# Performance work log

Measured on AMD Instinct MI355X. Metric: run time of the kernel, lower is better.

## Reference

```python
import jax, jax.numpy as jnp
import numpy as np

D_MODEL = 2048
D_STATE = 128
D_CONV = 4
EXPAND = 2
D_HEAD = 64
D_INNER = EXPAND * D_MODEL          # 4096 (= d_ssm, n_groups=1)
N_HEADS = D_INNER // D_HEAD         # 64
CONV_DIM = D_INNER + 2 * D_STATE    # 4352
D_IN_PROJ = 2 * D_INNER + 2 * D_STATE + N_HEADS  # 8512
CHUNK = 256
EPS = 1e-5


def setup_inputs() -> dict:
    key = jax.random.key(0)
    ks = jax.random.split(key, 8)
    B, L = 2, 4096
    u = jax.random.normal(ks[0], (B, L, D_MODEL), jnp.float32)
    W_in = 0.02 * jax.random.normal(ks[1], (D_IN_PROJ, D_MODEL), jnp.float32)
    conv_w = 0.1 * jax.random.normal(ks[2], (CONV_DIM, D_CONV), jnp.float32)
    conv_b = jnp.zeros((CONV_DIM,), jnp.float32)
    # dt_bias init: dt ~ exp(U*(log(.1)-log(.001)) + log(.001)); inv softplus
    dt = jnp.exp(jax.random.uniform(ks[3], (N_HEADS,)) * (np.log(0.1) - np.log(0.001)) + np.log(0.001))
    dt = jnp.clip(dt, 1e-4, None)
    dt_bias = dt + jnp.log(-jnp.expm1(-dt))
    A_log = jnp.log(jax.random.uniform(ks[4], (N_HEADS,), minval=1.0, maxval=16.0))
    Dp = jnp.ones((N_HEADS,), jnp.float32)
    norm_w = jnp.ones((D_INNER,), jnp.float32)
    W_out = 0.02 * jax.random.normal(ks[5], (D_MODEL, D_INNER), jnp.float32)
    return {"u": u, "W_in": W_in, "conv_w": conv_w, "conv_b": conv_b,
            "dt_bias": dt_bias, "A_log": A_log, "Dp": Dp, "norm_w": norm_w, "W_out": W_out}


def _forward(u, W_in, conv_w, conv_b, dt_bias, A_log, Dp, norm_w, W_out):
    b, l, _ = u.shape
    zxbcdt = u @ W_in.T                                   # [b,l,d_in_proj]
    z = zxbcdt[..., :D_INNER]                             # gate
    xBC = zxbcdt[..., D_INNER:D_INNER + CONV_DIM]
    dt = zxbcdt[..., D_INNER + CONV_DIM:]                 # [b,l,h]

    # depthwise causal conv1d + silu
    xpad = jnp.pad(xBC, ((0, 0), (D_CONV - 1, 0), (0, 0)))
    xBC = sum(xpad[:, w:w + l, :] * conv_w[:, w] for w in range(D_CONV)) + conv_b
    xBC = jax.nn.silu(xBC)

    x = xBC[..., :D_INNER]
    Bm = xBC[..., D_INNER:D_INNER + D_STATE]              # [b,l,n]
    Cm = xBC[..., D_INNER + D_STATE:]                     # [b,l,n]

    dt = jax.nn.softplus(dt + dt_bias)                    # [b,l,h]
    A = -jnp.exp(A_log)                                   # [h], negative

    c = l // CHUNK
    dtc = dt.reshape(b, c, CHUNK, h_ := N_HEADS)          # [b,c,s,h]
    dA_cs = jnp.cumsum(dtc * A, axis=2)                   # [b,c,s,h]
    xc = x.reshape(b, c, CHUNK, N_HEADS, D_HEAD)          # [b,c,s,h,p]
    Bc = Bm.reshape(b, c, CHUNK, D_STATE)                 # [b,c,s,n]
    Cc = Cm.reshape(b, c, CHUNK, D_STATE)

    # intra-chunk ("diagonal") term
    mask = jnp.tril(jnp.ones((CHUNK, CHUNK), bool))
    diff = dA_cs[:, :, :, None, :] - dA_cs[:, :, None, :, :]      # [b,c,i,j,h]
    L = jnp.exp(jnp.where(mask[None, None, :, :, None], diff, -jnp.inf))
    CB = jnp.einsum('bcin,bcjn->bcij', Cc, Bc)
    M = CB[..., None] * L * dtc[:, :, None, :, :]                 # [b,c,i,j,h]
    y_diag = jnp.einsum('bcijh,bcjhp->bcihp', M, xc)

    # per-chunk final states and inter-chunk scan
    decay_last = jnp.exp(dA_cs[:, :, -1:, :] - dA_cs)             # [b,c,s,h]
    states = jnp.einsum('bcsh,bcsn,bcshp->bchpn', decay_last * dtc, Bc, xc)
    chunk_decay = jnp.exp(dA_cs[:, :, -1, :])                     # [b,c,h]

    def step(s, inp):
        st, dec = inp
        return s * dec[:, :, None, None] + st, s

    s0 = jnp.zeros((b, N_HEADS, D_HEAD, D_STATE), u.dtype)
    _, prev = jax.lax.scan(step, s0, (states.transpose(1, 0, 2, 3, 4),
                                      chunk_decay.transpose(1, 0, 2)))
    prev = prev.transpose(1, 0, 2, 3, 4)                          # [b,c,h,p,n]

    y_off = jnp.einsum('bcin,bchpn,bcih->bcihp', Cc, prev, jnp.exp(dA_cs))

    y = y_diag + y_off + Dp[None, None, None, :, None] * xc       # [b,c,s,h,p]
    y = y.reshape(b, l, D_INNER)

    # gated RMSNorm (norm_before_gate=False): normalize(y * silu(z)) * w
    yg = y * jax.nn.silu(z)
    yg = yg * jax.lax.rsqrt(jnp.mean(yg * yg, axis=-1, keepdims=True) + EPS)
    y = yg * norm_w
    return y @ W_out.T                                            # [b,l,d_model]


def reference(u, W_in, conv_w, conv_b, dt_bias, A_log, Dp, norm_w, W_out):
    return _forward(u, W_in, conv_w, conv_b, dt_bias, A_log, Dp, norm_w, W_out)
```

## Files before the change

### kernel.cpp

```cpp
#include <hip/hip_runtime.h>
#include <hip/hip_bf16.h>

typedef long long ll;
typedef unsigned int uint;
typedef unsigned short ushort;

typedef __bf16 bf16x8 __attribute__((ext_vector_type(8)));
typedef float f32x4 __attribute__((ext_vector_type(4)));


__device__ __forceinline__ float silu_f(float x) { return x / (1.0f + expf(-x)); }
__device__ __forceinline__ float softplus_f(float x) {
  return x > 20.0f ? x : log1pf(expf(x));
}
__device__ __forceinline__ float b2f(ushort u) {
  return __uint_as_float(((uint)u) << 16);
}
__device__ __forceinline__ ushort f2b(float f) {
  uint x = __float_as_uint(f);
  return (ushort)((x + 0x7FFFu + ((x >> 16) & 1u)) >> 16);
}
__device__ __forceinline__ uint pk2(float a, float b) {
  return (uint)f2b(a) | ((uint)f2b(b) << 16);
}
__device__ __forceinline__ void unpack8(uint4 u, float* f) {
  f[0] = b2f((ushort)(u.x & 0xffff)); f[1] = b2f((ushort)(u.x >> 16));
  f[2] = b2f((ushort)(u.y & 0xffff)); f[3] = b2f((ushort)(u.y >> 16));
  f[4] = b2f((ushort)(u.z & 0xffff)); f[5] = b2f((ushort)(u.z >> 16));
  f[6] = b2f((ushort)(u.w & 0xffff)); f[7] = b2f((ushort)(u.w >> 16));
}
__device__ __forceinline__ void unpack8u(uint4 u, ushort* e) {
  e[0] = (ushort)(u.x & 0xffff); e[1] = (ushort)(u.x >> 16);
  e[2] = (ushort)(u.y & 0xffff); e[3] = (ushort)(u.y >> 16);
  e[4] = (ushort)(u.z & 0xffff); e[5] = (ushort)(u.z >> 16);
  e[6] = (ushort)(u.w & 0xffff); e[7] = (ushort)(u.w >> 16);
}

#define GLDS16(g, l)                                                     \
  __builtin_amdgcn_global_load_lds(                                      \
      (const __attribute__((address_space(1))) void*)(g),                \
      (__attribute__((address_space(3))) void*)(l), 16, 0, 0)

__global__ __launch_bounds__(256) void f32_to_bf16(
    const float* __restrict__ in, ushort* __restrict__ out, ll n)
{
  ll i = ((ll)blockIdx.x * 256 + threadIdx.x) * 8;
  if (i + 8 > n) return;
  float4 a = *(const float4*)&in[i];
  float4 b = *(const float4*)&in[i + 4];
  ushort4 o0; o0.x = f2b(a.x); o0.y = f2b(a.y); o0.z = f2b(a.z); o0.w = f2b(a.w);
  ushort4 o1; o1.x = f2b(b.x); o1.y = f2b(b.y); o1.z = f2b(b.z); o1.w = f2b(b.w);
  *(ushort4*)&out[i] = o0;
  *(ushort4*)&out[i + 4] = o1;
}

template <int CBF>
__global__ __launch_bounds__(256) void gemm_mfma(
    const ushort* __restrict__ A, const ushort* __restrict__ B, void* __restrict__ C,
    int Nreal, int K, int lda, int ldb, int ldc,
    ll batchA, ll batchB, ll batchC)
{
  A += (ll)blockIdx.z * batchA;
  B += (ll)blockIdx.z * batchB;
  __shared__ ushort As[128 * 32];
  __shared__ ushort Bs[128 * 32];
  const int t = threadIdx.x;
  const int lane = t & 63, w = t >> 6;
  const int wr = w >> 1, wc = w & 1;
  const int bm = blockIdx.y * 128, bn = blockIdx.x * 128;

  const int srow = t >> 2, skc = (t & 3) << 3;
  const ll a0 = (ll)(bm + srow) * lda + skc;
  const ll a1 = (ll)(bm + 64 + srow) * lda + skc;
  int br0 = bn + srow;      if (br0 >= Nreal) br0 = Nreal - 1;
  int br1 = bn + 64 + srow; if (br1 >= Nreal) br1 = Nreal - 1;
  const ll b0 = (ll)br0 * ldb + skc;
  const ll b1 = (ll)br1 * ldb + skc;
  ushort* lA0 = As + t * 8;        ushort* lA1 = As + 2048 + t * 8;
  ushort* lB0 = Bs + t * 8;        ushort* lB1 = Bs + 2048 + t * 8;

  f32x4 acc[4][4];
#pragma unroll
  for (int m = 0; m < 4; ++m)
#pragma unroll
    for (int n = 0; n < 4; ++n) acc[m][n] = (f32x4){0.f, 0.f, 0.f, 0.f};

  const int fr = lane & 15;
  const int fk = (lane >> 4) << 3;

  for (int k0 = 0; k0 < K; k0 += 32) {
    GLDS16(A + a0 + k0, lA0);
    GLDS16(A + a1 + k0, lA1);
    GLDS16(B + b0 + k0, lB0);
    GLDS16(B + b1 + k0, lB1);
    __syncthreads();
    bf16x8 af[4], bf[4];
#pragma unroll
    for (int m = 0; m < 4; ++m)
      af[m] = *(const bf16x8*)&As[(wr * 64 + m * 16 + fr) * 32 + fk];
#pragma unroll
    for (int n = 0; n < 4; ++n)
      bf[n] = *(const bf16x8*)&Bs[(wc * 64 + n * 16 + fr) * 32 + fk];
#pragma unroll
    for (int m = 0; m < 4; ++m)
#pragma unroll
      for (int n = 0; n < 4; ++n)
        acc[m][n] = __builtin_amdgcn_mfma_f32_16x16x32_bf16(af[m], bf[n], acc[m][n], 0, 0, 0);
    __syncthreads();
  }

  const int cr = (lane >> 4) << 2, cc = lane & 15;
  const ll zc = (ll)blockIdx.z * batchC;
#pragma unroll
  for (int m = 0; m < 4; ++m) {
#pragma unroll
    for (int n = 0; n < 4; ++n) {
#pragma unroll
      for (int j = 0; j < 4; ++j) {
        ll row = bm + wr * 64 + m * 16 + cr + j;
        int col = bn + wc * 64 + n * 16 + cc;
        if constexpr (CBF)
          ((ushort*)C)[zc + row * ldc + col] = f2b(acc[m][n][j]);
        else
          ((float*)C)[zc + row * ldc + col] = acc[m][n][j];
      }
    }
  }
}

__global__ __launch_bounds__(256) void conv_silu(
    const ushort* __restrict__ zx, const float* __restrict__ cw,
    const float* __restrict__ cbias, ushort* __restrict__ out)
{
  ll tid = (ll)blockIdx.x * 256 + threadIdx.x;
  int ch4 = (int)(tid % 1088) << 2;
  ll bl = tid / 1088;
  int l = (int)(bl & 4095);
  ll rowbase = bl - l;
  float4 acc = *(const float4*)&cbias[ch4];
  float4 w0 = *(const float4*)&cw[(ch4 + 0) * 4];
  float4 w1 = *(const float4*)&cw[(ch4 + 1) * 4];
  float4 w2 = *(const float4*)&cw[(ch4 + 2) * 4];
  float4 w3 = *(const float4*)&cw[(ch4 + 3) * 4];
#define TAP(W, COMP)                                                               \
  { int llx = l + (W) - 3;                                                         \
    if (llx >= 0) {                                                                \
      ushort4 xv = *(const ushort4*)&zx[(rowbase + llx) * 8576 + 4096 + ch4];      \
      acc.x = fmaf(b2f(xv.x), w0.COMP, acc.x);                                     \
      acc.y = fmaf(b2f(xv.y), w1.COMP, acc.y);                                     \
      acc.z = fmaf(b2f(xv.z), w2.COMP, acc.z);                                     \
      acc.w = fmaf(b2f(xv.w), w3.COMP, acc.w); } }
  TAP(0, x) TAP(1, y) TAP(2, z) TAP(3, w)
#undef TAP
  ushort4 o;
  o.x = f2b(silu_f(acc.x)); o.y = f2b(silu_f(acc.y));
  o.z = f2b(silu_f(acc.z)); o.w = f2b(silu_f(acc.w));
  *(ushort4*)&out[bl * 4352 + ch4] = o;
}

__global__ __launch_bounds__(256) void dt_cumsum(
    const ushort* __restrict__ zx, const float* __restrict__ dt_bias,
    const float* __restrict__ A_log, float* __restrict__ dt_sp,
    float* __restrict__ dA)
{
  __shared__ float sdt[256][64];
  const int bc = blockIdx.x;
  const int t = threadIdx.x;
#pragma unroll
  for (int q = 0; q < 16; ++q) {
    int ff = q * 256 + t;
    int i = ff >> 4;
    int h4 = (ff & 15) << 2;
    ushort4 v4 = *(const ushort4*)&zx[((ll)bc * 256 + i) * 8576 + 8448 + h4];
    float4 bb = *(const float4*)&dt_bias[h4];
    float4 v;
    v.x = softplus_f(b2f(v4.x) + bb.x); v.y = softplus_f(b2f(v4.y) + bb.y);
    v.z = softplus_f(b2f(v4.z) + bb.z); v.w = softplus_f(b2f(v4.w) + bb.w);
    *(float4*)&dt_sp[((ll)bc * 256 + i) * 64 + h4] = v;
    *(float4*)&sdt[i][h4] = v;
  }
  __syncthreads();
  if (t < 64) {
    const int h = t;
    const float Ah = -expf(A_log[h]);
    float run = 0.0f;
    for (int i = 0; i < 256; ++i) {
      run = fmaf(sdt[i][h], Ah, run);
      dA[((ll)bc * 256 + i) * 64 + h] = run;
    }
  }
}

__global__ __launch_bounds__(256) void bt_transpose(
    const ushort* __restrict__ xbc, ushort* __restrict__ BT)
{
  const int bc = blockIdx.x;
  const int st0 = blockIdx.y * 64;
  const int nt0 = blockIdx.z * 64;
  const int t = threadIdx.x;
  const int s_loc = t & 63, strip = t >> 6;
  const int nb = nt0 + strip * 16;
  const ll row = (ll)(bc * 256 + st0 + s_loc) * 4352 + 4096 + nb;
  uint4 v0 = *(const uint4*)&xbc[row];
  uint4 v1 = *(const uint4*)&xbc[row + 8];
  ushort e[16];
  unpack8u(v0, e); unpack8u(v1, e + 8);
#pragma unroll
  for (int k = 0; k < 16; ++k)
    BT[((ll)bc * 128 + nb + k) * 256 + st0 + s_loc] = e[k];
}

__global__ __launch_bounds__(256) void states_mfma(
    const ushort* __restrict__ xbc, const float* __restrict__ dt_sp,
    const float* __restrict__ dA, const ushort* __restrict__ BT,
    ushort* __restrict__ st)
{
  const int bc = blockIdx.x, h = blockIdx.y;
  const int t = threadIdx.x, lane = t & 63, w = t >> 6;
  __shared__ ushort xwT[64][264];
  const float dAl = dA[((ll)bc * 256 + 255) * 64 + h];
  const float wloc = expf(dAl - dA[((ll)bc * 256 + t) * 64 + h]) *
                     dt_sp[((ll)bc * 256 + t) * 64 + h];
  {
    const ll xrow = ((ll)bc * 256 + t) * 4352 + h * 64;
#pragma unroll
    for (int g = 0; g < 8; ++g) {
      uint4 v = *(const uint4*)&xbc[xrow + g * 8];
      float f[8]; unpack8(v, f);
#pragma unroll
      for (int j = 0; j < 8; ++j)
        xwT[g * 8 + j][t] = f2b(f[j] * wloc);
    }
  }
  __syncthreads();

  const int fr = lane & 15, fk = (lane >> 4) << 3;
  f32x4 acc[4][2];
#pragma unroll
  for (int m = 0; m < 4; ++m)
#pragma unroll
    for (int n = 0; n < 2; ++n) acc[m][n] = (f32x4){0.f, 0.f, 0.f, 0.f};

  for (int s0 = 0; s0 < 256; s0 += 32) {
    bf16x8 af[4], bf[2];
#pragma unroll
    for (int m = 0; m < 4; ++m)
      af[m] = *(const bf16x8*)&xwT[m * 16 + fr][s0 + fk];
#pragma unroll
    for (int n = 0; n < 2; ++n)
      bf[n] = *(const bf16x8*)&BT[((ll)bc * 128 + w * 32 + n * 16 + fr) * 256 + s0 + fk];
#pragma unroll
    for (int m = 0; m < 4; ++m)
#pragma unroll
      for (int n = 0; n < 2; ++n)
        acc[m][n] = __builtin_amdgcn_mfma_f32_16x16x32_bf16(af[m], bf[n], acc[m][n], 0, 0, 0);
  }

  const int cr = (lane >> 4) << 2, cc = lane & 15;
  const ll base = ((ll)bc * 64 + h) * 8192;
#pragma unroll
  for (int m = 0; m < 4; ++m)
#pragma unroll
    for (int n = 0; n < 2; ++n)
#pragma unroll
      for (int j = 0; j < 4; ++j) {
        int p = m * 16 + cr + j;
        int nn = w * 32 + n * 16 + cc;
        st[base + p * 128 + nn] = f2b(acc[m][n][j]);
      }
}

__global__ __launch_bounds__(256) void scan_kernel(
    ushort* __restrict__ st, const float* __restrict__ dA)
{
  ll tid = (ll)blockIdx.x * 256 + threadIdx.x;
  int n = (int)(tid & 127);
  int p = (int)((tid >> 7) & 63);
  int h = (int)((tid >> 13) & 63);
  int b = (int)(tid >> 19);
  float s = 0.0f;
#pragma unroll
  for (int c = 0; c < 16; ++c) {
    int bc = b * 16 + c;
    float dec = expf(dA[((ll)bc * 256 + 255) * 64 + h]);
    ll idx = ((ll)bc * 64 + h) * 8192 + p * 128 + n;
    float tmp = b2f(st[idx]);
    st[idx] = f2b(s);
    s = fmaf(s, dec, tmp);
  }
}

__global__ __launch_bounds__(256) void ssm_y_mfma(
    const ushort* __restrict__ xbc, const float* __restrict__ dt_sp,
    const float* __restrict__ dA, const ushort* __restrict__ CB,
    const ushort* __restrict__ prev, const float* __restrict__ Dp,
    ushort* __restrict__ zx)
{
  const int bc = blockIdx.x, h = blockIdx.y;
  const int t = threadIdx.x, lane = t & 63, w = t >> 6;
  __shared__ float sA[256], sdt[256];
  __shared__ ushort xT[64][264];
  __shared__ ushort pv[64][136];

  sA[t]  = dA[((ll)bc * 256 + t) * 64 + h];
  sdt[t] = dt_sp[((ll)bc * 256 + t) * 64 + h];
  {
    const ll xrow = ((ll)bc * 256 + t) * 4352 + h * 64;
#pragma unroll
    for (int g = 0; g < 8; ++g) {
      uint4 v = *(const uint4*)&xbc[xrow + g * 8];
      ushort e[8]; unpack8u(v, e);
#pragma unroll
      for (int j = 0; j < 8; ++j) xT[g * 8 + j][t] = e[j];
    }
  }
  {
    const int p = t >> 2, n0 = (t & 3) * 32;
    const ll pb = ((ll)bc * 64 + h) * 8192 + (ll)p * 128 + n0;
#pragma unroll
    for (int g = 0; g < 4; ++g)
      *(uint4*)&pv[p][n0 + g * 8] = *(const uint4*)&prev[pb + g * 8];
  }
  __syncthreads();

  const int fr = lane & 15, fk = (lane >> 4) << 3;
  float dAi[4], ei[4];
  int im[4];
#pragma unroll
  for (int m = 0; m < 4; ++m) {
    im[m] = w * 64 + m * 16 + fr;
    dAi[m] = sA[im[m]];
    ei[m] = __expf(dAi[m]);
  }

  f32x4 acc[4][4];
#pragma unroll
  for (int m = 0; m < 4; ++m)
#pragma unroll
    for (int n = 0; n < 4; ++n) acc[m][n] = (f32x4){0.f, 0.f, 0.f, 0.f};

  const int nsteps = 2 * w + 2;
  for (int js = 0; js < nsteps; ++js) {
    const int j0 = js * 32;
    bf16x8 bf[4];
#pragma unroll
    for (int n = 0; n < 4; ++n)
      bf[n] = *(const bf16x8*)&xT[n * 16 + fr][j0 + fk];
    bf16x8 af[4];
#pragma unroll
    for (int m = 0; m < 4; ++m) {
      uint4 cb4 = *(const uint4*)&CB[((ll)bc * 256 + im[m]) * 256 + j0 + fk];
      float cb[8]; unpack8(cb4, cb);
#pragma unroll
      for (int jj = 0; jj < 8; ++jj) {
        int j = j0 + fk + jj;
        float mv = cb[jj] * sdt[j] * __expf(dAi[m] - sA[j]);
        af[m][jj] = (__bf16)((j <= im[m]) ? mv : 0.0f);
      }
    }
#pragma unroll
    for (int m = 0; m < 4; ++m)
#pragma unroll
      for (int n = 0; n < 4; ++n)
        acc[m][n] = __builtin_amdgcn_mfma_f32_16x16x32_bf16(af[m], bf[n], acc[m][n], 0, 0, 0);
  }

  for (int ns = 0; ns < 4; ++ns) {
    const int n0 = ns * 32;
    bf16x8 bf[4];
#pragma unroll
    for (int n = 0; n < 4; ++n)
      bf[n] = *(const bf16x8*)&pv[n * 16 + fr][n0 + fk];
    bf16x8 af[4];
#pragma unroll
    for (int m = 0; m < 4; ++m) {
      uint4 cv4 = *(const uint4*)&xbc[((ll)bc * 256 + im[m]) * 4352 + 4224 + n0 + fk];
      float cv[8]; unpack8(cv4, cv);
#pragma unroll
      for (int jj = 0; jj < 8; ++jj)
        af[m][jj] = (__bf16)(cv[jj] * ei[m]);
    }
#pragma unroll
    for (int m = 0; m < 4; ++m)
#pragma unroll
      for (int n = 0; n < 4; ++n)
        acc[m][n] = __builtin_amdgcn_mfma_f32_16x16x32_bf16(af[m], bf[n], acc[m][n], 0, 0, 0);
  }

  const int cr = (lane >> 4) << 2, cc = lane & 15;
  const float dph = Dp[h];
#pragma unroll
  for (int m = 0; m < 4; ++m) {
#pragma unroll
    for (int n = 0; n < 4; ++n) {
#pragma unroll
      for (int j = 0; j < 4; ++j) {
        int i_loc = w * 64 + m * 16 + cr + j;
        int p = n * 16 + cc;
        float xval = b2f(xT[p][i_loc]);
        float val = acc[m][n][j] + dph * xval;
        zx[((ll)bc * 256 + i_loc) * 8576 + 4096 + h * 64 + p] = f2b(val);
      }
    }
  }
}

__global__ __launch_bounds__(256) void gated_rmsnorm(
    ushort* __restrict__ zx, const float* __restrict__ norm_w)
{
  const ll row = blockIdx.x;
  ushort* zrow = zx + row * 8576;
  ushort* yrow = zrow + 4096;
  const int t = threadIdx.x;
  float g[16];
  float ss = 0.0f;
#pragma unroll
  for (int q = 0; q < 2; ++q) {
    int d = q * 2048 + t * 8;
    uint4 yv = *(const uint4*)&yrow[d];
    uint4 zv = *(const uint4*)&zrow[d];
    float yf[8], zf[8];
    unpack8(yv, yf);
    unpack8(zv, zf);
#pragma unroll
    for (int j = 0; j < 8; ++j) {
      float gv = yf[j] * silu_f(zf[j]);
      g[q * 8 + j] = gv;
      ss += gv * gv;
    }
  }
#pragma unroll
  for (int o = 32; o > 0; o >>= 1) ss += __shfl_xor(ss, o);
  __shared__ float red[4];
  if ((t & 63) == 0) red[t >> 6] = ss;
  __syncthreads();
  ss = red[0] + red[1] + red[2] + red[3];
  float scale = rsqrtf(ss * (1.0f / 4096.0f) + 1e-5f);
#pragma unroll
  for (int q = 0; q < 2; ++q) {
    int d = q * 2048 + t * 8;
    float4 w0 = *(const float4*)&norm_w[d];
    float4 w1 = *(const float4*)&norm_w[d + 4];
    uint4 o;
    o.x = pk2(g[q * 8 + 0] * scale * w0.x, g[q * 8 + 1] * scale * w0.y);
    o.y = pk2(g[q * 8 + 2] * scale * w0.z, g[q * 8 + 3] * scale * w0.w);
    o.z = pk2(g[q * 8 + 4] * scale * w1.x, g[q * 8 + 5] * scale * w1.y);
    o.w = pk2(g[q * 8 + 6] * scale * w1.z, g[q * 8 + 7] * scale * w1.w);
    *(uint4*)&yrow[d] = o;
  }
}

extern "C" void kernel_launch(void* const* d_in, const int* in_sizes, int n_in,
                              void* d_out, int out_size, void* d_ws, size_t ws_size,
                              hipStream_t stream) {
  const float* u       = (const float*)d_in[0];
  const float* W_in    = (const float*)d_in[1];
  const float* conv_w  = (const float*)d_in[2];
  const float* conv_b  = (const float*)d_in[3];
  const float* dt_bias = (const float*)d_in[4];
  const float* A_log   = (const float*)d_in[5];
  const float* Dp      = (const float*)d_in[6];
  const float* norm_w  = (const float*)d_in[7];
  const float* W_out   = (const float*)d_in[8];
  float* out = (float*)d_out;

  char* wsb = (char*)d_ws;
  ushort* zx      = (ushort*)wsb;
  ushort* xbc     = (ushort*)(wsb + 140509184LL);
  ushort* u_bf    = xbc;
  ushort* Win_bf  = (ushort*)(wsb + 174063616LL);
  ushort* st      = (ushort*)(wsb + 211812352LL);
  ushort* Wout_bf = st;
  ushort* CBb     = (ushort*)(wsb + 245366784LL);
  float*  dt_sp   = (float*)(wsb + 249561088LL);
  float*  dAcs    = (float*)(wsb + 251658240LL);
  ushort* BT      = (ushort*)(wsb + 253755392LL);

  f32_to_bf16<<<8192, 256, 0, stream>>>(u, u_bf, 16777216LL);
  f32_to_bf16<<<8512, 256, 0, stream>>>(W_in, Win_bf, 17432576LL);
  gemm_mfma<1><<<dim3(67, 64), 256, 0, stream>>>(
      u_bf, Win_bf, zx, 8512, 2048, 2048, 2048, 8576, 0, 0, 0);
  conv_silu<<<34816, 256, 0, stream>>>(zx, conv_w, conv_b, xbc);
  dt_cumsum<<<32, 256, 0, stream>>>(zx, dt_bias, A_log, dt_sp, dAcs);
  bt_transpose<<<dim3(32, 4, 2), 256, 0, stream>>>(xbc, BT);
  gemm_mfma<1><<<dim3(2, 2, 32), 256, 0, stream>>>(
      xbc + 4224, xbc + 4096, CBb, 256, 128, 4352, 4352, 256,
      256LL * 4352, 256LL * 4352, 65536LL);
  states_mfma<<<dim3(32, 64), 256, 0, stream>>>(xbc, dt_sp, dAcs, BT, st);
  scan_kernel<<<4096, 256, 0, stream>>>(st, dAcs);
  ssm_y_mfma<<<dim3(32, 64), 256, 0, stream>>>(xbc, dt_sp, dAcs, CBb, st, Dp, zx);
  gated_rmsnorm<<<8192, 256, 0, stream>>>(zx, norm_w);
  f32_to_bf16<<<4096, 256, 0, stream>>>(W_out, Wout_bf, 8388608LL);
  gemm_mfma<0><<<dim3(16, 64), 256, 0, stream>>>(
      zx + 4096, Wout_bf, out, 2048, 4096, 8576, 4096, 2048, 0, 0, 0);
}
```

Before: 1.110 ms.

## Replace projection GEMMs with 256x256-tile 512-thread MFMA kernel using swizzled LDS

Adds a new GEMM kernel with 256x256 output tiles, 8 waves per block, double-buffered direct global-to-LDS loads with an XOR-swizzled layout, and a grouped block-index remap for L2 locality. It replaces the 128x128 GEMM used for both the input and output projections. Larger tiles raise arithmetic intensity and cut global traffic per FLOP. The trade-off is higher register pressure (32 accumulator vectors per wave) and fewer blocks, which can hurt occupancy and tail balance, especially for the output GEMM with only 256 blocks.

```diff
diff --git a/kernel.cpp b/kernel.cpp
--- a/kernel.cpp
+++ b/kernel.cpp
@@ -52,6 +52,112 @@
   ushort4 o1; o1.x = f2b(b.x); o1.y = f2b(b.y); o1.z = f2b(b.z); o1.w = f2b(b.w);
   *(ushort4*)&out[i] = o0;
   *(ushort4*)&out[i + 4] = o1;
+}
+
+template <int CBF>
+__global__ __launch_bounds__(512, 2) void gemm256(
+    const ushort* __restrict__ A, const ushort* __restrict__ B, void* __restrict__ C,
+    int Nreal, int Nstore, int K, int lda, int ldb, int ldc, int gx)
+{
+  __shared__ ushort lds[2][2][8192];
+  const int t = threadIdx.x;
+  const int lane = t & 63, w = t >> 6;
+  const int wm = w >> 2, wn = w & 3;
+
+  const int nwg = gridDim.x;
+  const int bid = blockIdx.x;
+  const int swz = (bid & 7) * (nwg >> 3) + (bid >> 3);
+  const int bm = (swz / gx) * 256, bn = (swz % gx) * 256;
+
+  ll ga0, ga1, gb0, gb1;
+  {
+    int G0 = t, G1 = 512 + t;
+    int r0 = G0 >> 2, r1 = G1 >> 2;
+    int s0 = (G0 & 3) ^ (r0 & 3), s1 = (G1 & 3) ^ (r1 & 3);
+    ga0 = (ll)(bm + r0) * lda + s0 * 8;
+    ga1 = (ll)(bm + r1) * lda + s1 * 8;
+    int br0 = bn + r0; if (br0 >= Nreal) br0 = Nreal - 1;
+    int br1 = bn + r1; if (br1 >= Nreal) br1 = Nreal - 1;
+    gb0 = (ll)br0 * ldb + s0 * 8;
+    gb1 = (ll)br1 * ldb + s1 * 8;
+  }
+#define STAGE256(buf, k0) do {                        \
+    GLDS16(A + ga0 + (k0), &lds[buf][0][t * 8]);      \
+    GLDS16(A + ga1 + (k0), &lds[buf][0][t * 8 + 4096]); \
+    GLDS16(B + gb0 + (k0), &lds[buf][1][t * 8]);      \
+    GLDS16(B + gb1 + (k0), &lds[buf][1][t * 8 + 4096]); \
+  } while (0)
+
+  f32x4 acc[8][4];
+#pragma unroll
+  for (int m = 0; m < 8; ++m)
+#pragma unroll
+    for (int n = 0; n < 4; ++n) acc[m][n] = (f32x4){0.f, 0.f, 0.f, 0.f};
+
+  const int fr = lane & 15, q = lane >> 4;
+  int aoff[8], boff[4];
+#pragma unroll
+  for (int m = 0; m < 8; ++m) {
+    int r = wm * 128 + m * 16 + fr;
+    aoff[m] = r * 32 + ((q ^ (r & 3)) << 3);
+  }
+#pragma unroll
+  for (int n = 0; n < 4; ++n) {
+    int r = wn * 64 + n * 16 + fr;
+    boff[n] = r * 32 + ((q ^ (r & 3)) << 3);
+  }
+
+  const int NT = K >> 5;
+  STAGE256(0, 0);
+  STAGE256(1, 32);
+  asm volatile("s_waitcnt vmcnt(4)" ::: "memory");
+  asm volatile("s_barrier" ::: "memory");
+
+  for (int kt = 0; kt < NT; ++kt) {
+    const int cur = kt & 1;
+    bf16x8 af[8], bf[4];
+#pragma unroll
+    for (int m = 0; m < 8; ++m) af[m] = *(const bf16x8*)&lds[cur][0][aoff[m]];
+#pragma unroll
+    for (int n = 0; n < 4; ++n) bf[n] = *(const bf16x8*)&lds[cur][1][boff[n]];
+    __builtin_amdgcn_s_setprio(1);
+#pragma unroll
+    for (int m = 0; m < 8; ++m)
+#pragma unroll
+      for (int n = 0; n < 4; ++n)
+        acc[m][n] = __builtin_amdgcn_mfma_f32_16x16x32_bf16(af[m], bf[n], acc[m][n], 0, 0, 0);
+    __builtin_amdgcn_s_setprio(0);
+    if (kt + 1 < NT) {
+      asm volatile("s_barrier" ::: "memory");
+      if (kt + 2 < NT) {
+        STAGE256(cur, (kt + 2) * 32);
+        asm volatile("s_waitcnt vmcnt(4)" ::: "memory");
+      } else {
+        asm volatile("s_waitcnt vmcnt(0)" ::: "memory");
+      }
+      asm volatile("s_barrier" ::: "memory");
+    }
+  }
+#undef STAGE256
+
+  const int cr = (lane >> 4) << 2, cc = lane & 15;
+#pragma unroll
+  for (int m = 0; m < 8; ++m) {
+#pragma unroll
+    for (int n = 0; n < 4; ++n) {
+#pragma unroll
+      for (int j = 0; j < 4; ++j) {
+        ll row = bm + wm * 128 + m * 16 + cr + j;
+        int col = bn + wn * 64 + n * 16 + cc;
+        if (col < Nstore) {
+          if constexpr (CBF)
+            ((ushort*)C)[row * ldc + col] = f2b(acc[m][n][j]);
+          else
+            ((float*)C)[row * ldc + col] = acc[m][n][j];
+        }
+      }
+    }
+  }
 }
 
 template <int CBF>
@@ -478,8 +584,8 @@
 
   f32_to_bf16<<<8192, 256, 0, stream>>>(u, u_bf, 16777216LL);
   f32_to_bf16<<<8512, 256, 0, stream>>>(W_in, Win_bf, 17432576LL);
-  gemm_mfma<1><<<dim3(67, 64), 256, 0, stream>>>(
-      u_bf, Win_bf, zx, 8512, 2048, 2048, 2048, 8576, 0, 0, 0);
+  gemm256<1><<<1088, 512, 0, stream>>>(
+      u_bf, Win_bf, zx, 8512, 8576, 2048, 2048, 2048, 8576, 34);
   conv_silu<<<34816, 256, 0, stream>>>(zx, conv_w, conv_b, xbc);
   dt_cumsum<<<32, 256, 0, stream>>>(zx, dt_bias, A_log, dt_sp, dAcs);
   bt_transpose<<<dim3(32, 4, 2), 256, 0, stream>>>(xbc, BT);
@@ -491,6 +597,6 @@
   ssm_y_mfma<<<dim3(32, 64), 256, 0, stream>>>(xbc, dt_sp, dAcs, CBb, st, Dp, zx);
   gated_rmsnorm<<<8192, 256, 0, stream>>>(zx, norm_w);
   f32_to_bf16<<<4096, 256, 0, stream>>>(W_out, Wout_bf, 8388608LL);
-  gemm_mfma<0><<<dim3(16, 64), 256, 0, stream>>>(
-      zx + 4096, Wout_bf, out, 2048, 4096, 8576, 4096, 2048, 0, 0, 0);
-}
+  gemm256<0><<<256, 512, 0, stream>>>(
+      zx + 4096, Wout_bf, out, 2048, 2048, 4096, 8576, 4096, 2048, 8);
+}
```

Result: faster. 964.6 us (-13.1%).
